# Kernel tuning notes

Measured on AMD Instinct MI355X. Metric: run time of the kernel, lower is better.

The kernel has to match this reference:

```python
import jax, jax.numpy as jnp
import numpy as np

HID, STEM, BN_OUT, STEM_OUT, MLP = 256, 64, 128, 64, 128
BN_WS, STEM_WS = 5, 17
N, H_BN, W_BN, H_VIS, W_VIS = 4096, 128, 128, 1024, 1024


def setup_inputs() -> dict:
    key = jax.random.key(0)
    ks = jax.random.split(key, 24)
    f32 = jnp.float32
    def rn(k, shape, s=0.05):
        return jax.random.normal(k, shape, f32) * s
    return dict(
        bottleneck=rn(ks[0], (1, HID, H_BN, W_BN), 1.0),
        vis_stem_features=rn(ks[1], (1, STEM, H_VIS, W_VIS), 1.0),
        source_positions_vis=jax.random.uniform(ks[2], (N, 2), f32, 10.0, W_VIS - 10.0),
        pixel_to_sky=rn(ks[3], (N, 2, 2), 0.1),
        fused_h=H_BN, fused_w=W_BN, vis_h=H_VIS, vis_w=W_VIS,
        dw_w=rn(ks[4], (HID, 1, 7, 7)), dw_b=rn(ks[5], (HID,)),
        ln_g=jnp.ones((HID,), f32), ln_b=jnp.zeros((HID,), f32),
        pw1_w=rn(ks[6], (4 * HID, HID)), pw1_b=rn(ks[7], (4 * HID,)),
        pw2_w=rn(ks[8], (HID, 4 * HID)), pw2_b=rn(ks[9], (HID,)),
        cn_gamma=jnp.full((HID,), 1e-2, f32),
        bn1x1_w=rn(ks[10], (BN_OUT, HID, 1, 1)), bn1x1_b=rn(ks[11], (BN_OUT,)),
        st1_w=rn(ks[12], (STEM_OUT, STEM, 3, 3)), st1_b=rn(ks[13], (STEM_OUT,)),
        st2_w=rn(ks[14], (STEM_OUT, STEM_OUT, 3, 3)), st2_b=rn(ks[15], (STEM_OUT,)),
        h1_w=rn(ks[16], (MLP, BN_OUT + STEM_OUT)), h1_b=rn(ks[17], (MLP,)),
        h2_w=rn(ks[18], (MLP, MLP)), h2_b=rn(ks[19], (MLP,)),
        h3_w=rn(ks[20], (3, MLP)),
        h3_b=jnp.array([0.0, 0.0, float(np.log(0.05))], f32),
    )


def _gelu(x):
    return jax.nn.gelu(x, approximate=False)


def _conv2d(x, w, b, padding, groups=1):
    y = jax.lax.conv_general_dilated(
        x, w, (1, 1), [(padding, padding), (padding, padding)],
        dimension_numbers=('NCHW', 'OIHW', 'NCHW'), feature_group_count=groups)
    return y + b[None, :, None, None]


def _bilinear_windows(fm, pos, ws):
    """fm [1,C,H,W], pos [N,2] pixel coords -> [N,C,ws,ws].
    Matches torch grid_sample(mode=bilinear, padding=zeros, align_corners=True)
    with the module's normalize/unnormalize, i.e. direct pixel-coord sampling."""
    C, H, W = fm.shape[1:]
    fm2 = fm[0]
    half = ws // 2
    off = jnp.arange(-half, half + 1, dtype=pos.dtype)
    gy, gx = jnp.meshgrid(off, off, indexing='ij')
    xs = gx[None] + pos[:, 0, None, None]   # [N,ws,ws]
    ys = gy[None] + pos[:, 1, None, None]
    x0 = jnp.floor(xs); y0 = jnp.floor(ys)
    wx1 = xs - x0; wy1 = ys - y0
    x0i = x0.astype(jnp.int32); y0i = y0.astype(jnp.int32)
    def gather(yi, xi, w):
        valid = (yi >= 0) & (yi < H) & (xi >= 0) & (xi < W)
        v = fm2[:, jnp.clip(yi, 0, H - 1), jnp.clip(xi, 0, W - 1)]  # [C,N,ws,ws]
        return v * (w * valid)[None]
    out = (gather(y0i, x0i, (1 - wy1) * (1 - wx1))
           + gather(y0i, x0i + 1, (1 - wy1) * wx1)
           + gather(y0i + 1, x0i, wy1 * (1 - wx1))
           + gather(y0i + 1, x0i + 1, wy1 * wx1))
    return jnp.transpose(out, (1, 0, 2, 3))


def _gauss(ws):
    t = jnp.linspace(-1.0, 1.0, ws)
    yy, xx = jnp.meshgrid(t, t, indexing='ij')
    g = jnp.exp(-(xx ** 2 + yy ** 2) / (2 * 0.4 ** 2))
    return g / g.sum()


def _convnext(x, dw_w, dw_b, ln_g, ln_b, pw1_w, pw1_b, pw2_w, pw2_b, gamma):
    r = x
    x = _conv2d(x, dw_w, dw_b, padding=3, groups=x.shape[1])  # depthwise 7x7
    mu = x.mean(1, keepdims=True)
    var = ((x - mu) ** 2).mean(1, keepdims=True)
    x = (x - mu) / jnp.sqrt(var + 1e-6)
    x = x * ln_g[None, :, None, None] + ln_b[None, :, None, None]
    x = jnp.einsum('nchw,oc->nohw', x, pw1_w) + pw1_b[None, :, None, None]
    x = _gelu(x)
    x = jnp.einsum('nchw,oc->nohw', x, pw2_w) + pw2_b[None, :, None, None]
    return r + gamma[None, :, None, None] * x


def _forward(bottleneck, vis_stem_features, source_positions_vis, pixel_to_sky,
             dw_w, dw_b, ln_g, ln_b, pw1_w, pw1_b, pw2_w, pw2_b, cn_gamma,
             bn1x1_w, bn1x1_b, st1_w, st1_b, st2_w, st2_b,
             h1_w, h1_b, h2_w, h2_b, h3_w, h3_b,
             fused_h, fused_w, vis_h, vis_w):
    scale = jnp.array([fused_w / vis_w, fused_h / vis_h], source_positions_vis.dtype)
    pos_bn = source_positions_vis * scale
    # bottleneck branch: 5x5 windows -> ConvNeXt -> 1x1 conv -> GELU -> gauss pool
    bn_win = _bilinear_windows(bottleneck, pos_bn, BN_WS)              # [N,256,5,5]
    bn_feat = _convnext(bn_win, dw_w, dw_b, ln_g, ln_b, pw1_w, pw1_b, pw2_w, pw2_b, cn_gamma)
    bn_feat = _gelu(_conv2d(bn_feat, bn1x1_w, bn1x1_b, padding=0))     # [N,128,5,5]
    bn_vec = (bn_feat * _gauss(BN_WS)[None, None]).sum((-2, -1))       # [N,128]
    st_win = _bilinear_windows(vis_stem_features, source_positions_vis, STEM_WS)
    st = _gelu(_conv2d(st_win, st1_w, st1_b, padding=1))
    st = _gelu(_conv2d(st, st2_w, st2_b, padding=1))                   # [N,64,17,17]
    st_vec = (st * _gauss(STEM_WS)[None, None]).sum((-2, -1))          # [N,64]
    # head MLP
    x = jnp.concatenate([bn_vec, st_vec], axis=1)                      # [N,192]
    x = _gelu(x @ h1_w.T + h1_b)
    x = _gelu(x @ h2_w.T + h2_b)
    out = x @ h3_w.T + h3_b                                            # [N,3]
    dx_px, dy_px = out[:, 0], out[:, 1]
    log_sigma = jnp.clip(out[:, 2], -6.0, 3.0)
    pix = jnp.stack([dx_px, dy_px], axis=1)                            # [N,2]
    pred_sky = jnp.einsum('nij,nj->ni', pixel_to_sky, pix)             # [N,2]
    confidence = 1.0 / jnp.maximum(jnp.exp(log_sigma), 1e-4)
    return pred_sky, dx_px, dy_px, log_sigma, confidence


def reference(bottleneck, vis_stem_features, source_positions_vis, pixel_to_sky,
              fused_h, fused_w, vis_h, vis_w,
              dw_w, dw_b, ln_g, ln_b, pw1_w, pw1_b, pw2_w, pw2_b, cn_gamma,
              bn1x1_w, bn1x1_b, st1_w, st1_b, st2_w, st2_b,
              h1_w, h1_b, h2_w, h2_b, h3_w, h3_b):
    return _forward(bottleneck, vis_stem_features, source_positions_vis, pixel_to_sky,
                    dw_w, dw_b, ln_g, ln_b, pw1_w, pw1_b, pw2_w, pw2_b, cn_gamma,
                    bn1x1_w, bn1x1_b, st1_w, st1_b, st2_w, st2_b,
                    h1_w, h1_b, h2_w, h2_b, h3_w, h3_b,
                    fused_h, fused_w, vis_h, vis_w)
```

## Files before the change

### kernel.cpp

```cpp
#include <hip/hip_runtime.h>
#include <hip/hip_bf16.h>

#define XSTR 28

typedef short short8 __attribute__((ext_vector_type(8)));
typedef float f32x4  __attribute__((ext_vector_type(4)));
typedef float f32x16 __attribute__((ext_vector_type(16)));

__device__ __forceinline__ float gelu_f(float x){
    return 0.5f*x*(1.0f + erff(x*0.70710678118654752f));
}
__device__ __forceinline__ float gelu_q(float x){
    const float z = 1.5957691216057308f*x*(1.0f + 0.044715f*x*x);
    return x / (1.0f + __expf(-z));
}
__device__ __forceinline__ unsigned short f2bf(float f){
    unsigned int u = __float_as_uint(f);
    u += 0x7fffu + ((u>>16)&1u);
    return (unsigned short)(u>>16);
}
__device__ __forceinline__ unsigned int pack2(float a, float b){
    return (unsigned int)f2bf(a) | ((unsigned int)f2bf(b)<<16);
}
__device__ __forceinline__ float bf_lo(unsigned int u){ return __uint_as_float(u<<16); }
__device__ __forceinline__ float bf_hi(unsigned int u){ return __uint_as_float(u & 0xffff0000u); }
__device__ __forceinline__ float bfu(unsigned short v){ return __uint_as_float(((unsigned int)v)<<16); }

__device__ __forceinline__ void fma_row25(const float* __restrict__ row, float w, float* __restrict__ acc){
    const float4* r4 = (const float4*)row;
    float4 a0=r4[0], a1=r4[1], a2=r4[2], a3=r4[3], a4=r4[4], a5=r4[5];
    float a6 = row[24];
    acc[0]+=a0.x*w;  acc[1]+=a0.y*w;  acc[2]+=a0.z*w;  acc[3]+=a0.w*w;
    acc[4]+=a1.x*w;  acc[5]+=a1.y*w;  acc[6]+=a1.z*w;  acc[7]+=a1.w*w;
    acc[8]+=a2.x*w;  acc[9]+=a2.y*w;  acc[10]+=a2.z*w; acc[11]+=a2.w*w;
    acc[12]+=a3.x*w; acc[13]+=a3.y*w; acc[14]+=a3.z*w; acc[15]+=a3.w*w;
    acc[16]+=a4.x*w; acc[17]+=a4.y*w; acc[18]+=a4.z*w; acc[19]+=a4.w*w;
    acc[20]+=a5.x*w; acc[21]+=a5.y*w; acc[22]+=a5.z*w; acc[23]+=a5.w*w;
    acc[24]+=a6*w;
}

__device__ __forceinline__ void bn_body(
    unsigned char* __restrict__ U, int n0, int t,
    const float* __restrict__ bottleneck, const float* __restrict__ pos,
    const float* __restrict__ dw_w, const float* __restrict__ dw_b,
    const float* __restrict__ ln_g, const float* __restrict__ ln_b,
    const float* __restrict__ pw1_b, const float* __restrict__ pw2_b,
    const float* __restrict__ cn_gamma, const float* __restrict__ bn1x1_b,
    const short8* __restrict__ P1v, const short8* __restrict__ P2v,
    const short8* __restrict__ Pbv,
    float* __restrict__ vec_out)
{
    unsigned char* Xb = U;
    unsigned char* Hc = U + 32768;
    float* redA = (float*)(U + 49152);
    float* redB = (float*)(U + 50752);
    float* muS  = (float*)(U + 52352);
    float* rsS  = (float*)(U + 52576);

    const int lane = t & 63, w = t >> 6;
    const int mcol = lane & 15, h4 = lane >> 4;
    const int sP = t >> 8, cP = t & 255;

    unsigned int wvp[13];
    float xdw[25];
    {
        const int n = n0 + sP;
        const float px = pos[2*n]*0.125f, py = pos[2*n+1]*0.125f;
        const float fpx = floorf(px), fpy = floorf(py);
        const int ix0 = (int)fpx - 2, iy0 = (int)fpy - 2;
        const float fx = px - fpx, fy = py - fpy;
        const float w00=(1.f-fy)*(1.f-fx), w01=(1.f-fy)*fx, w10=fy*(1.f-fx), w11=fy*fx;
        float wv[25];
        {
            const float* fm = bottleneck + cP*16384;
            float P[6][6];
            #pragma unroll
            for (int r=0;r<6;r++){
                const int y = iy0+r;
                const bool yok = (y>=0)&&(y<128);
                const int yc = y<0?0:(y>127?127:y);
                #pragma unroll
                for (int s=0;s<6;s++){
                    const int x = ix0+s;
                    const bool ok = yok && (x>=0) && (x<128);
                    const int xc = x<0?0:(x>127?127:x);
                    P[r][s] = ok ? fm[yc*128+xc] : 0.f;
                }
            }
            #pragma unroll
            for (int a=0;a<5;a++)
            #pragma unroll
            for (int b=0;b<5;b++)
                wv[a*5+b] = w00*P[a][b]+w01*P[a][b+1]+w10*P[a+1][b]+w11*P[a+1][b+1];
        }
        #pragma unroll
        for (int i=0;i<12;i++) wvp[i] = pack2(wv[2*i], wv[2*i+1]);
        wvp[12] = pack2(wv[24], 0.f);
        {
            float wcr[49];
            const float* wc = dw_w + cP*49;
            #pragma unroll
            for (int k=0;k<49;k++) wcr[k]=wc[k];
            const float bb = dw_b[cP];
            #pragma unroll
            for (int i=0;i<5;i++){
                #pragma unroll
                for (int j=0;j<5;j++){
                    float a = bb;
                    #pragma unroll
                    for (int u=0;u<7;u++){
                        const int y = i+u-3;
                        if (y<0||y>4) continue;
                        #pragma unroll
                        for (int v=0;v<7;v++){
                            const int x = j+v-3;
                            if (x<0||x>4) continue;
                            a += wv[y*5+x]*wcr[u*7+v];
                        }
                    }
                    xdw[i*5+j] = a;
                }
            }
        }
        #pragma unroll
        for (int p=0;p<25;p++){
            const int row = sP*32 + p;
            *(unsigned short*)(Xb + row*512 + ((2*cP) ^ ((row&7)<<4))) = f2bf(xdw[p]);
        }
    }
    __syncthreads();
    if (t < 400){
        const int sp = t>>3, part = t&7;
        const int row = (sp/25)*32 + (sp - (sp/25)*25);
        float a=0.f, b=0.f;
        for (int c=part; c<256; c+=8){
            const float v = bfu(*(const unsigned short*)(Xb + row*512 + ((2*c) ^ ((row&7)<<4))));
            a += v; b += v*v;
        }
        redA[t]=a; redB[t]=b;
    }
    __syncthreads();
    if (t < 50){
        float a=0.f, b=0.f;
        #pragma unroll
        for (int s=0;s<8;s++){ a+=redA[t*8+s]; b+=redB[t*8+s]; }
        const float m = a*(1.f/256.f);
        const float var = b*(1.f/256.f) - m*m;
        muS[t]=m; rsS[t]=rsqrtf(var+1e-6f);
    }
    __syncthreads();
    {
        const float g = ln_g[cP], bb = ln_b[cP];
        #pragma unroll
        for (int p=0;p<25;p++){
            const int row = sP*32 + p;
            const float v = (xdw[p]-muS[sP*25+p])*rsS[sP*25+p]*g + bb;
            *(unsigned short*)(Xb + row*512 + ((2*cP) ^ ((row&7)<<4))) = f2bf(v);
        }
    }
    __syncthreads();

    f32x4 acc2[2][4];
    #pragma unroll
    for (int ml=0;ml<2;ml++)
        #pragma unroll
        for (int nt=0;nt<4;nt++) acc2[ml][nt]=0.f;

    for (int ch=0; ch<8; ++ch){
        const int mt = ch*8 + w;
        f32x4 a1[4];
        #pragma unroll
        for (int nt=0;nt<4;nt++) a1[nt]=0.f;
        #pragma unroll
        for (int kk=0; kk<8; ++kk){
            const short8 av = P1v[((mt<<3)+kk)*64 + lane];
            #pragma unroll
            for (int nt=0; nt<4; ++nt){
                const int row = nt*16 + mcol;
                const int ad = row*512 + ((kk*64 + h4*16) ^ ((row&7)<<4));
                const short8 bv = *(const short8*)(Xb + ad);
                a1[nt] = __builtin_amdgcn_mfma_f32_16x16x32_bf16(av, bv, a1[nt], 0,0,0);
            }
        }
        {
            const float4 b1v = *(const float4*)(pw1_b + mt*16 + h4*4);
            #pragma unroll
            for (int nt=0; nt<4; ++nt){
                const int row = nt*16 + mcol;
                const float g0 = gelu_q(a1[nt].x + b1v.x);
                const float g1 = gelu_q(a1[nt].y + b1v.y);
                const float g2 = gelu_q(a1[nt].z + b1v.z);
                const float g3 = gelu_q(a1[nt].w + b1v.w);
                const int ad = row*256 + ((w*32 + h4*8) ^ ((row&7)<<4));
                *(uint2*)(Hc + ad) = make_uint2(pack2(g0,g1), pack2(g2,g3));
            }
        }
        __syncthreads();
        #pragma unroll
        for (int ml=0; ml<2; ++ml){
            const int mtc = w*2 + ml;
            #pragma unroll
            for (int kk2=0; kk2<4; ++kk2){
                const short8 av = P2v[(mtc*32 + (ch*4 + kk2))*64 + lane];
                #pragma unroll
                for (int nt=0; nt<4; ++nt){
                    const int row = nt*16 + mcol;
                    const int ad = row*256 + ((kk2*64 + h4*16) ^ ((row&7)<<4));
                    const short8 bv = *(const short8*)(Hc + ad);
                    acc2[ml][nt] = __builtin_amdgcn_mfma_f32_16x16x32_bf16(av, bv, acc2[ml][nt], 0,0,0);
                }
            }
        }
        __syncthreads();
    }

    #pragma unroll
    for (int ml=0; ml<2; ++ml){
        const int c0 = (w*2+ml)*16 + h4*4;
        const float4 gm = *(const float4*)(cn_gamma + c0);
        const float4 b2 = *(const float4*)(pw2_b + c0);
        #pragma unroll
        for (int nt=0; nt<4; ++nt){
            const int row = nt*16 + mcol;
            const int ad = row*512 + ((2*c0) ^ ((row&7)<<4));
            const float f0 = gm.x*(acc2[ml][nt].x + b2.x);
            const float f1 = gm.y*(acc2[ml][nt].y + b2.y);
            const float f2 = gm.z*(acc2[ml][nt].z + b2.z);
            const float f3 = gm.w*(acc2[ml][nt].w + b2.w);
            *(uint2*)(Xb + ad) = make_uint2(pack2(f0,f1), pack2(f2,f3));
        }
    }
    __syncthreads();
    #pragma unroll
    for (int p=0;p<25;p++){
        const int row = sP*32 + p;
        unsigned short* ptr = (unsigned short*)(Xb + row*512 + ((2*cP) ^ ((row&7)<<4)));
        const float r = (p&1) ? bf_hi(wvp[p>>1]) : bf_lo(wvp[p>>1]);
        *ptr = f2bf(bfu(*ptr) + r);
    }
    __syncthreads();

    {
        f32x4 a3[4];
        #pragma unroll
        for (int nt=0;nt<4;nt++) a3[nt]=0.f;
        #pragma unroll
        for (int kk=0; kk<8; ++kk){
            const short8 av = Pbv[((w<<3)+kk)*64 + lane];
            #pragma unroll
            for (int nt=0; nt<4; ++nt){
                const int row = nt*16 + mcol;
                const int ad = row*512 + ((kk*64 + h4*16) ^ ((row&7)<<4));
                const short8 bv = *(const short8*)(Xb + ad);
                a3[nt] = __builtin_amdgcn_mfma_f32_16x16x32_bf16(av, bv, a3[nt], 0,0,0);
            }
        }
        const float4 bb = *(const float4*)(bn1x1_b + w*16 + h4*4);
        float e5[5];
        #pragma unroll
        for (int a=0;a<5;a++){
            const float ta = -1.f + 0.5f*a;
            e5[a] = expf(-3.125f*ta*ta);
        }
        const float Sv = e5[0]+e5[1]+e5[2]+e5[3]+e5[4];
        const float invS = 1.0f/(Sv*Sv);
        float sA[2][4];
        #pragma unroll
        for (int s=0;s<2;s++)
            #pragma unroll
            for (int j=0;j<4;j++) sA[s][j]=0.f;
        #pragma unroll
        for (int nt=0; nt<4; ++nt){
            const int row = nt*16 + mcol;
            const int s = row>>5, p = row&31;
            if (p < 25){
                const int pa = p/5, pb = p - pa*5;
                const float g = e5[pa]*e5[pb];
                sA[s][0] += g*gelu_q(a3[nt].x + bb.x);
                sA[s][1] += g*gelu_q(a3[nt].y + bb.y);
                sA[s][2] += g*gelu_q(a3[nt].z + bb.z);
                sA[s][3] += g*gelu_q(a3[nt].w + bb.w);
            }
        }
        #pragma unroll
        for (int off=1; off<16; off<<=1){
            #pragma unroll
            for (int s=0;s<2;s++)
                #pragma unroll
                for (int j=0;j<4;j++) sA[s][j] += __shfl_xor(sA[s][j], off);
        }
        if (mcol == 0){
            const int o = w*16 + h4*4;
            #pragma unroll
            for (int s=0;s<2;s++){
                float* vo = vec_out + (n0+s)*192 + o;
                vo[0]=sA[s][0]*invS; vo[1]=sA[s][1]*invS;
                vo[2]=sA[s][2]*invS; vo[3]=sA[s][3]*invS;
            }
        }
    }
}

#define STEM_CONV32(SRC, AP)                                                        \
    _Pragma("unroll")                                                               \
    for (int k=0;k<9;k++){                                                          \
        int tj[3];                                                                  \
        _Pragma("unroll")                                                           \
        for (int j=0;j<3;j++)                                                       \
            tj[j] = (int)sTab[m*90 + (j<cnt ? st+j : st)*9 + k];                    \
        _Pragma("unroll")                                                           \
        for (int kt=0;kt<4;kt++){                                                   \
            const short8 av = (AP)[(k*8 + kt*2 + wo)*64 + lane];                    \
            const int cb = kt*32 + hi16;                                            \
            _Pragma("unroll")                                                       \
            for (int j=0;j<3;j++){                                                  \
                if (j < cnt){                                                       \
                    const short8 bv = *(const short8*)((SRC) + (tj[j] ^ cb));       \
                    acc[j] = __builtin_amdgcn_mfma_f32_32x32x16_bf16(av, bv, acc[j], 0,0,0); \
                }                                                                   \
            }                                                                       \
        }                                                                           \
    }

__device__ __forceinline__ void stem_body(
    unsigned char* __restrict__ U, int n, int t,
    const float* __restrict__ vis, const float* __restrict__ pos,
    const short8* __restrict__ Ap1,
    const float* __restrict__ st1_b, const float* __restrict__ st2_b,
    float* __restrict__ vec_out)
{
    unsigned char* sXt = U;
    unsigned short* sTab = (unsigned short*)(U + 37120);
    float (*redS)[4] = (float(*)[4])(U + 42880);

    const int lane = t & 63;
    const int m = lane & 31;
    const int hi = lane >> 5;
    const int hi16 = hi*16;
    const int w = t >> 6;
    const int wo = w & 1;
    const int nh = w >> 1;
    const int st  = nh*3 - (nh==3 ? 1 : 0);
    const int cnt = (nh < 2) ? 3 : 2;

    const float fpx0 = pos[2*n], fpy0 = pos[2*n+1];
    const float fpx = floorf(fpx0), fpy = floorf(fpy0);
    const int ix0 = (int)fpx - 8, iy0 = (int)fpy - 8;
    const float fx = fpx0-fpx, fy = fpy0-fpy;
    const float w00=(1.f-fy)*(1.f-fx), w01=(1.f-fy)*fx, w10=fy*(1.f-fx), w11=fy*fx;

    if (t < 32) *(unsigned int*)(sXt + 289*128 + t*4) = 0u;

    for (int idx = t; idx < 32*90; idx += 512){
        const int mm = idx/90, rem = idx - mm*90;
        const int nt = rem/9, k = rem - nt*9;
        const int p = nt*32 + mm;
        int pp = 289;
        if (p < 289){
            const int py = (p*241)>>12, px = p - py*17;
            const int y = py + k/3 - 1, x = px + (k - (k/3)*3) - 1;
            if (((unsigned)y < 17u) && ((unsigned)x < 17u)) pp = y*17 + x;
        }
        sTab[idx] = (unsigned short)(pp*128 + ((pp&7)<<4));
    }

    for (int task = t; task < 64*17; task += 512){
        const int c  = task & 63;
        const int py = task >> 6;
        const float* r0 = vis + c*1048576 + (iy0+py)*1024 + ix0;
        float a[18], b[18];
        #pragma unroll
        for (int kk=0; kk<18; kk++){ a[kk]=r0[kk]; b[kk]=r0[1024+kk]; }
        #pragma unroll
        for (int px=0; px<17; px++){
            const float v = w00*a[px] + w01*a[px+1] + w10*b[px] + w11*b[px+1];
            const int p = py*17 + px;
            *(unsigned short*)(sXt + p*128 + ((2*c) ^ ((p&7)<<4))) = f2bf(v);
        }
    }
    __syncthreads();

    f32x16 acc[3];
    #pragma unroll
    for (int j=0;j<3;j++) acc[j] = 0.f;
    STEM_CONV32(sXt, Ap1)

    uint2 pk[3][4];
    {
        float4 b4[4];
        #pragma unroll
        for (int rg=0;rg<4;rg++) b4[rg] = *(const float4*)(st1_b + wo*32 + 8*rg + 4*hi);
        #pragma unroll
        for (int j=0;j<3;j++){
            if (j < cnt){
                #pragma unroll
                for (int rg=0;rg<4;rg++){
                    const float v0 = gelu_q(acc[j][4*rg+0] + b4[rg].x);
                    const float v1 = gelu_q(acc[j][4*rg+1] + b4[rg].y);
                    const float v2 = gelu_q(acc[j][4*rg+2] + b4[rg].z);
                    const float v3 = gelu_q(acc[j][4*rg+3] + b4[rg].w);
                    pk[j][rg] = make_uint2(pack2(v0,v1), pack2(v2,v3));
                }
            }
        }
    }
    __syncthreads();

    #pragma unroll
    for (int j=0;j<3;j++){
        if (j < cnt){
            const int p = (st+j)*32 + m;
            if (p < 289){
                const int swz = (p&7)<<4;
                #pragma unroll
                for (int rg=0;rg<4;rg++){
                    const int ch0 = wo*32 + 8*rg + 4*hi;
                    *(uint2*)(sXt + p*128 + ((2*ch0) ^ swz)) = pk[j][rg];
                }
            }
        }
    }
    __syncthreads();

    const short8* Ap2 = Ap1 + 4608;
    #pragma unroll
    for (int j=0;j<3;j++) acc[j] = 0.f;
    STEM_CONV32(sXt, Ap2)

    {
        float4 b4[4];
        #pragma unroll
        for (int rg=0;rg<4;rg++) b4[rg] = *(const float4*)(st2_b + wo*32 + 8*rg + 4*hi);
        float s[16];
        #pragma unroll
        for (int r=0;r<16;r++) s[r]=0.f;
        #pragma unroll
        for (int j=0;j<3;j++){
            if (j < cnt){
                const int p = (st+j)*32 + m;
                if (p < 289){
                    const int py = (p*241)>>12;
                    const int px = p - py*17;
                    const float ty = -1.f + 0.125f*py;
                    const float tx = -1.f + 0.125f*px;
                    const float g = expf(-3.125f*(ty*ty + tx*tx));
                    #pragma unroll
                    for (int rg=0;rg<4;rg++){
                        s[4*rg+0] += g*gelu_q(acc[j][4*rg+0] + b4[rg].x);
                        s[4*rg+1] += g*gelu_q(acc[j][4*rg+1] + b4[rg].y);
                        s[4*rg+2] += g*gelu_q(acc[j][4*rg+2] + b4[rg].z);
                        s[4*rg+3] += g*gelu_q(acc[j][4*rg+3] + b4[rg].w);
                    }
                }
            }
        }
        #pragma unroll
        for (int off=1; off<32; off<<=1){
            #pragma unroll
            for (int r=0;r<16;r++) s[r] += __shfl_xor(s[r], off);
        }
        if (m == 0){
            #pragma unroll
            for (int rg=0;rg<4;rg++)
                #pragma unroll
                for (int e=0;e<4;e++)
                    redS[wo*32 + 8*rg + 4*hi + e][nh] = s[4*rg+e];
        }
    }
    __syncthreads();
    if (t < 64){
        float Sv = 0.f;
        #pragma unroll
        for (int j=0;j<17;j++){
            const float tj = -1.f + 0.125f*j;
            Sv += expf(-3.125f*tj*tj);
        }
        vec_out[n*192+128+t] = (redS[t][0] + redS[t][1] + redS[t][2] + redS[t][3]) / (Sv*Sv);
    }
}

__global__ __launch_bounds__(512,4) void fused_branches(
    const float* __restrict__ bottleneck, const float* __restrict__ vis,
    const float* __restrict__ pos,
    const float* __restrict__ dw_w, const float* __restrict__ dw_b,
    const float* __restrict__ ln_g, const float* __restrict__ ln_b,
    const float* __restrict__ pw1_b, const float* __restrict__ pw2_b,
    const float* __restrict__ cn_gamma, const float* __restrict__ bn1x1_b,
    const short8* __restrict__ P1v, const short8* __restrict__ P2v,
    const short8* __restrict__ Pbv,
    const short8* __restrict__ Ap1,
    const float* __restrict__ st1_b, const float* __restrict__ st2_b,
    float* __restrict__ vec_out)
{
    __shared__ __align__(16) unsigned char U[52800];
    const int b = blockIdx.x, t = threadIdx.x;
    const int q = b/3, r = b - q*3;
    if (r == 0){
        bn_body(U, q*2, t, bottleneck, pos, dw_w, dw_b, ln_g, ln_b,
                pw1_b, pw2_b, cn_gamma, bn1x1_b, P1v, P2v, Pbv, vec_out);
    } else {
        stem_body(U, q*2 + r - 1, t, vis, pos, Ap1, st1_b, st2_b, vec_out);
    }
}

__global__ __launch_bounds__(256) void prepack_bn_kernel(
    const float* __restrict__ W1, const float* __restrict__ W2, const float* __restrict__ Wb,
    unsigned short* __restrict__ P1, unsigned short* __restrict__ P2, unsigned short* __restrict__ Pb)
{
    const int tid = blockIdx.x*256 + threadIdx.x;
    const float* src; unsigned short* dst; int row, col, stride, idx;
    if (tid < 32768){
        idx = tid;
        const int frag = idx>>6, l = idx&63;
        row = (frag>>3)*16 + (l&15); col = (frag&7)*32 + (l>>4)*8; stride = 256;
        src = W1; dst = P1;
    } else if (tid < 65536){
        idx = tid - 32768;
        const int frag = idx>>6, l = idx&63;
        row = (frag>>5)*16 + (l&15); col = (frag&31)*32 + (l>>4)*8; stride = 1024;
        src = W2; dst = P2;
    } else if (tid < 69632){
        idx = tid - 65536;
        const int frag = idx>>6, l = idx&63;
        row = (frag>>3)*16 + (l&15); col = (frag&7)*32 + (l>>4)*8; stride = 256;
        src = Wb; dst = Pb;
    } else return;
    const float* s = src + row*stride + col;
    unsigned int v[4];
    #pragma unroll
    for (int j=0;j<4;j++) v[j] = pack2(s[2*j], s[2*j+1]);
    *(uint4*)(dst + (size_t)idx*8) = make_uint4(v[0],v[1],v[2],v[3]);
}

__global__ __launch_bounds__(256,2) void bn_branch_valu(
    const float* __restrict__ bottleneck, const float* __restrict__ pos,
    const float* __restrict__ dw_w, const float* __restrict__ dw_b,
    const float* __restrict__ ln_g, const float* __restrict__ ln_b,
    const float* __restrict__ pw1_w, const float* __restrict__ pw1_b,
    const float* __restrict__ pw2_w, const float* __restrict__ pw2_b,
    const float* __restrict__ cn_gamma,
    const float* __restrict__ bn1x1_w, const float* __restrict__ bn1x1_b,
    float* __restrict__ vec_out)
{
    __shared__ float xln[256*XSTR];
    __shared__ float hbuf[256*XSTR];
    __shared__ float redA[200], redB[200];
    __shared__ float mu[25], rs[25];

    const int n = blockIdx.x;
    const int t = threadIdx.x;
    const int c = t;

    const float px = pos[2*n]*0.125f, py = pos[2*n+1]*0.125f;
    const float fpx = floorf(px), fpy = floorf(py);
    const int ix0 = (int)fpx - 2, iy0 = (int)fpy - 2;
    const float fx = px - fpx, fy = py - fpy;
    const float w00=(1.f-fy)*(1.f-fx), w01=(1.f-fy)*fx, w10=fy*(1.f-fx), w11=fy*fx;

    float wv[25];
    {
        const float* fm = bottleneck + c*16384;
        float P[6][6];
        #pragma unroll
        for (int r=0;r<6;r++){
            const int y = iy0+r;
            const bool yok = (y>=0)&&(y<128);
            const int yc = y<0?0:(y>127?127:y);
            #pragma unroll
            for (int s=0;s<6;s++){
                const int x = ix0+s;
                const bool ok = yok && (x>=0) && (x<128);
                const int xc = x<0?0:(x>127?127:x);
                P[r][s] = ok ? fm[yc*128+xc] : 0.f;
            }
        }
        #pragma unroll
        for (int a=0;a<5;a++)
        #pragma unroll
        for (int b=0;b<5;b++)
            wv[a*5+b] = w00*P[a][b]+w01*P[a][b+1]+w10*P[a+1][b]+w11*P[a+1][b+1];
    }
    {
        float wcr[49];
        const float* wc = dw_w + c*49;
        #pragma unroll
        for (int k=0;k<49;k++) wcr[k]=wc[k];
        const float bb = dw_b[c];
        #pragma unroll
        for (int i=0;i<5;i++){
            #pragma unroll
            for (int j=0;j<5;j++){
                float a = bb;
                #pragma unroll
                for (int u=0;u<7;u++){
                    const int y = i+u-3;
                    if (y<0||y>4) continue;
                    #pragma unroll
                    for (int v=0;v<7;v++){
                        const int x = j+v-3;
                        if (x<0||x>4) continue;
                        a += wv[y*5+x]*wcr[u*7+v];
                    }
                }
                xln[c*XSTR + i*5+j] = a;
            }
        }
    }
    __syncthreads();
    if (t < 200){
        const int p = t>>3, s = t&7;
        float a=0.f, b=0.f;
        for (int cc=s; cc<256; cc+=8){
            const float v = xln[cc*XSTR+p];
            a += v; b += v*v;
        }
        redA[t]=a; redB[t]=b;
    }
    __syncthreads();
    if (t < 25){
        float a=0.f, b=0.f;
        #pragma unroll
        for (int s=0;s<8;s++){ a+=redA[t*8+s]; b+=redB[t*8+s]; }
        const float m = a*(1.f/256.f);
        const float var = b*(1.f/256.f) - m*m;
        mu[t]=m; rs[t]=rsqrtf(var+1e-6f);
    }
    __syncthreads();
    {
        const float g = ln_g[c], bb = ln_b[c];
        #pragma unroll
        for (int p=0;p<25;p++)
            xln[c*XSTR+p] = (xln[c*XSTR+p]-mu[p])*rs[p]*g + bb;
    }
    __syncthreads();
    float acc2[25];
    #pragma unroll
    for (int p=0;p<25;p++) acc2[p]=0.f;
    for (int r=0;r<4;r++){
        const int o = r*256 + t;
        float h[25];
        {
            const float b1 = pw1_b[o];
            #pragma unroll
            for (int p=0;p<25;p++) h[p]=b1;
            const float* wr = pw1_w + o*256;
            for (int cc=0;cc<256;cc++)
                fma_row25(xln + cc*XSTR, wr[cc], h);
            #pragma unroll
            for (int p=0;p<25;p++) h[p]=gelu_f(h[p]);
        }
        __syncthreads();
        #pragma unroll
        for (int p=0;p<25;p++) hbuf[t*XSTR+p]=h[p];
        __syncthreads();
        {
            const float* w2 = pw2_w + t*1024 + r*256;
            for (int k=0;k<256;k++)
                fma_row25(hbuf + k*XSTR, w2[k], acc2);
        }
    }
    {
        const float gam = cn_gamma[c], b2 = pw2_b[c];
        #pragma unroll
        for (int p=0;p<25;p++)
            xln[c*XSTR+p] = wv[p] + gam*(acc2[p]+b2);
    }
    __syncthreads();
    if (t < 128){
        float acc[25];
        #pragma unroll
        for (int p=0;p<25;p++) acc[p]=0.f;
        const float* wr = bn1x1_w + t*256;
        for (int cc=0;cc<256;cc++)
            fma_row25(xln + cc*XSTR, wr[cc], acc);
        const float b = bn1x1_b[t];
        float e5[5];
        #pragma unroll
        for (int a=0;a<5;a++){
            const float ta = -1.f + 0.5f*a;
            e5[a] = expf(-3.125f*ta*ta);
        }
        const float Sv = e5[0]+e5[1]+e5[2]+e5[3]+e5[4];
        float res = 0.f;
        #pragma unroll
        for (int a=0;a<5;a++){
            float rowa = 0.f;
            #pragma unroll
            for (int bb=0;bb<5;bb++)
                rowa += e5[bb]*gelu_f(acc[a*5+bb]+b);
            res += e5[a]*rowa;
        }
        vec_out[n*192+t] = res/(Sv*Sv);
    }
}

__global__ __launch_bounds__(256) void prepack_kernel(
    const float* __restrict__ W1, const float* __restrict__ W2,
    unsigned short* __restrict__ Ap)
{
    const int tid = blockIdx.x*256 + threadIdx.x;
    if (tid >= 9216) return;
    const int conv = tid / 4608;
    const int r = tid - conv*4608;
    const int frag = r >> 6, l = r & 63;
    const int k  = frag >> 3;
    const int kt = (frag >> 1) & 3;
    const int wo = frag & 1;
    const float* W = conv ? W2 : W1;
    const int o  = wo*32 + (l & 31);
    const int c0 = kt*16 + (l >> 5)*8;
    unsigned int v[4];
    #pragma unroll
    for (int jj=0; jj<4; jj++){
        const float f0 = W[o*576 + (c0+2*jj  )*9 + k];
        const float f1 = W[o*576 + (c0+2*jj+1)*9 + k];
        v[jj] = pack2(f0, f1);
    }
    *(uint4*)(Ap + (size_t)tid*8) = make_uint4(v[0], v[1], v[2], v[3]);
}

__global__ __launch_bounds__(512,4) void stem_branch_kernel(
    const float* __restrict__ vis,
    const float* __restrict__ pos,
    const short8* __restrict__ Ap1,
    const float* __restrict__ st1_b,
    const float* __restrict__ st2_b,
    float* __restrict__ vec_out)
{
    __shared__ __align__(16) unsigned char U[43904];
    stem_body(U, blockIdx.x, threadIdx.x, vis, pos, Ap1, st1_b, st2_b, vec_out);
}

__global__ __launch_bounds__(128) void head16_kernel(
    const float* __restrict__ vec, const float* __restrict__ p2s,
    const float* __restrict__ h1_w, const float* __restrict__ h1_b,
    const float* __restrict__ h2_w, const float* __restrict__ h2_b,
    const float* __restrict__ h3_w, const float* __restrict__ h3_b,
    float* __restrict__ out, int N)
{
    __shared__ float v[16][192];
    __shared__ float x1s[16][132];
    __shared__ float x2s[16][132];
    __shared__ float o3s[16][4];
    const int n0 = blockIdx.x*16, t = threadIdx.x;

    for (int idx=t; idx<16*192; idx+=128){
        const int s = idx/192, k = idx - s*192;
        v[s][k] = vec[n0*192 + idx];
    }
    __syncthreads();
    {
        const int o = t;
        float acc[16];
        const float b = h1_b[o];
        #pragma unroll
        for (int s=0;s<16;s++) acc[s]=b;
        const float4* wr = (const float4*)(h1_w + o*192);
        for (int k4=0;k4<48;k4++){
            const float4 wv4 = wr[k4];
            #pragma unroll
            for (int s=0;s<16;s++){
                const float4 vv = *(const float4*)&v[s][k4*4];
                acc[s] += wv4.x*vv.x + wv4.y*vv.y + wv4.z*vv.z + wv4.w*vv.w;
            }
        }
        #pragma unroll
        for (int s=0;s<16;s++) x1s[s][o] = gelu_f(acc[s]);
    }
    __syncthreads();
    {
        const int o = t;
        float acc[16];
        const float b = h2_b[o];
        #pragma unroll
        for (int s=0;s<16;s++) acc[s]=b;
        const float4* wr = (const float4*)(h2_w + o*128);
        for (int k4=0;k4<32;k4++){
            const float4 wv4 = wr[k4];
            #pragma unroll
            for (int s=0;s<16;s++){
                const float4 vv = *(const float4*)&x1s[s][k4*4];
                acc[s] += wv4.x*vv.x + wv4.y*vv.y + wv4.z*vv.z + wv4.w*vv.w;
            }
        }
        #pragma unroll
        for (int s=0;s<16;s++) x2s[s][o] = gelu_f(acc[s]);
    }
    __syncthreads();
    if (t < 48){
        const int j = t>>4, s = t&15;
        float a = h3_b[j];
        const float* wr = h3_w + j*128;
        for (int k=0;k<128;k++) a += x2s[s][k]*wr[k];
        o3s[s][j] = a;
    }
    __syncthreads();
    if (t < 16){
        const int s = t, n = n0 + s;
        const float dx = o3s[s][0], dy = o3s[s][1];
        float ls = o3s[s][2];
        ls = ls < -6.f ? -6.f : (ls > 3.f ? 3.f : ls);
        const float s0 = p2s[n*4+0]*dx + p2s[n*4+1]*dy;
        const float s1 = p2s[n*4+2]*dx + p2s[n*4+3]*dy;
        const float conf = 1.0f/fmaxf(expf(ls), 1e-4f);
        out[2*n]   = s0;
        out[2*n+1] = s1;
        out[2*N+n] = dx;
        out[3*N+n] = dy;
        out[4*N+n] = ls;
        out[5*N+n] = conf;
    }
}

extern "C" void kernel_launch(void* const* d_in, const int* in_sizes, int n_in,
                              void* d_out, int out_size, void* d_ws, size_t ws_size,
                              hipStream_t stream)
{
    (void)n_in; (void)out_size;
    const float* bottleneck = (const float*)d_in[0];
    const float* vis        = (const float*)d_in[1];
    const float* pos        = (const float*)d_in[2];
    const float* p2s        = (const float*)d_in[3];
    const float* dw_w  = (const float*)d_in[8];
    const float* dw_b  = (const float*)d_in[9];
    const float* ln_g  = (const float*)d_in[10];
    const float* ln_b  = (const float*)d_in[11];
    const float* pw1_w = (const float*)d_in[12];
    const float* pw1_b = (const float*)d_in[13];
    const float* pw2_w = (const float*)d_in[14];
    const float* pw2_b = (const float*)d_in[15];
    const float* gam   = (const float*)d_in[16];
    const float* b1w   = (const float*)d_in[17];
    const float* b1b   = (const float*)d_in[18];
    const float* s1w   = (const float*)d_in[19];
    const float* s1b   = (const float*)d_in[20];
    const float* s2w   = (const float*)d_in[21];
    const float* s2b   = (const float*)d_in[22];
    const float* h1w   = (const float*)d_in[23];
    const float* h1b   = (const float*)d_in[24];
    const float* h2w   = (const float*)d_in[25];
    const float* h2b   = (const float*)d_in[26];
    const float* h3w   = (const float*)d_in[27];
    const float* h3b   = (const float*)d_in[28];

    const int N = in_sizes[2]/2;
    float* vec = (float*)d_ws;
    const size_t vec_bytes = (size_t)N*192*sizeof(float);
    unsigned short* Apack = (unsigned short*)((char*)d_ws + vec_bytes);
    unsigned short* P1 = Apack + 73728;
    unsigned short* P2 = P1 + 262144;
    unsigned short* Pb = P2 + 262144;
    const size_t need = vec_bytes + 147456u + (262144u+262144u+32768u)*2u;

    hipMemsetAsync(d_ws, 0, vec_bytes, stream);

    prepack_kernel<<<36, 256, 0, stream>>>(s1w, s2w, Apack);

    if (ws_size >= need){
        prepack_bn_kernel<<<272, 256, 0, stream>>>(pw1_w, pw2_w, b1w, P1, P2, Pb);
        fused_branches<<<3*(N/2), 512, 0, stream>>>(bottleneck, vis, pos,
                                                    dw_w, dw_b, ln_g, ln_b,
                                                    pw1_b, pw2_b, gam, b1b,
                                                    (const short8*)P1, (const short8*)P2, (const short8*)Pb,
                                                    (const short8*)Apack, s1b, s2b, vec);
    } else {
        bn_branch_valu<<<N, 256, 0, stream>>>(bottleneck, pos, dw_w, dw_b, ln_g, ln_b,
                                              pw1_w, pw1_b, pw2_w, pw2_b, gam, b1w, b1b, vec);
        stem_branch_kernel<<<N, 512, 0, stream>>>(vis, pos, (const short8*)Apack, s1b, s2b, vec);
    }
    head16_kernel<<<N/16, 128, 0, stream>>>(vec, p2s, h1w, h1b, h2w, h2b, h3w, h3b,
                                            (float*)d_out, N);
}
```

Before: 869.3 us.

## Pre-transpose vis stem features to channel-last bf16 and split fused kernel

Adds a kernel that converts the full 64x1024x1024 vis feature map into a channel-last bf16 copy, so each stem block gathers its 17x17 bilinear window with 16-byte vector loads instead of strided per-channel fp32 reads. The combined bottleneck/stem launch is split back into separate stem and bottleneck kernels. The trade is an extra full-map pass (256MB read, 128MB write) and a 128MB workspace requirement; the fast path only runs if the workspace is large enough. Bilinear inputs are now bf16-rounded before interpolation, which adds a little rounding error.

```diff
diff --git a/kernel.cpp b/kernel.cpp
--- a/kernel.cpp
+++ b/kernel.cpp
@@ -301,206 +301,19 @@
     }
 }
 
-#define STEM_CONV32(SRC, AP)                                                        \
-    _Pragma("unroll")                                                               \
-    for (int k=0;k<9;k++){                                                          \
-        int tj[3];                                                                  \
-        _Pragma("unroll")                                                           \
-        for (int j=0;j<3;j++)                                                       \
-            tj[j] = (int)sTab[m*90 + (j<cnt ? st+j : st)*9 + k];                    \
-        _Pragma("unroll")                                                           \
-        for (int kt=0;kt<4;kt++){                                                   \
-            const short8 av = (AP)[(k*8 + kt*2 + wo)*64 + lane];                    \
-            const int cb = kt*32 + hi16;                                            \
-            _Pragma("unroll")                                                       \
-            for (int j=0;j<3;j++){                                                  \
-                if (j < cnt){                                                       \
-                    const short8 bv = *(const short8*)((SRC) + (tj[j] ^ cb));       \
-                    acc[j] = __builtin_amdgcn_mfma_f32_32x32x16_bf16(av, bv, acc[j], 0,0,0); \
-                }                                                                   \
-            }                                                                       \
-        }                                                                           \
-    }
-
-__device__ __forceinline__ void stem_body(
-    unsigned char* __restrict__ U, int n, int t,
-    const float* __restrict__ vis, const float* __restrict__ pos,
-    const short8* __restrict__ Ap1,
-    const float* __restrict__ st1_b, const float* __restrict__ st2_b,
-    float* __restrict__ vec_out)
-{
-    unsigned char* sXt = U;
-    unsigned short* sTab = (unsigned short*)(U + 37120);
-    float (*redS)[4] = (float(*)[4])(U + 42880);
-
-    const int lane = t & 63;
-    const int m = lane & 31;
-    const int hi = lane >> 5;
-    const int hi16 = hi*16;
-    const int w = t >> 6;
-    const int wo = w & 1;
-    const int nh = w >> 1;
-    const int st  = nh*3 - (nh==3 ? 1 : 0);
-    const int cnt = (nh < 2) ? 3 : 2;
-
-    const float fpx0 = pos[2*n], fpy0 = pos[2*n+1];
-    const float fpx = floorf(fpx0), fpy = floorf(fpy0);
-    const int ix0 = (int)fpx - 8, iy0 = (int)fpy - 8;
-    const float fx = fpx0-fpx, fy = fpy0-fpy;
-    const float w00=(1.f-fy)*(1.f-fx), w01=(1.f-fy)*fx, w10=fy*(1.f-fx), w11=fy*fx;
-
-    if (t < 32) *(unsigned int*)(sXt + 289*128 + t*4) = 0u;
-
-    for (int idx = t; idx < 32*90; idx += 512){
-        const int mm = idx/90, rem = idx - mm*90;
-        const int nt = rem/9, k = rem - nt*9;
-        const int p = nt*32 + mm;
-        int pp = 289;
-        if (p < 289){
-            const int py = (p*241)>>12, px = p - py*17;
-            const int y = py + k/3 - 1, x = px + (k - (k/3)*3) - 1;
-            if (((unsigned)y < 17u) && ((unsigned)x < 17u)) pp = y*17 + x;
-        }
-        sTab[idx] = (unsigned short)(pp*128 + ((pp&7)<<4));
-    }
-
-    for (int task = t; task < 64*17; task += 512){
-        const int c  = task & 63;
-        const int py = task >> 6;
-        const float* r0 = vis + c*1048576 + (iy0+py)*1024 + ix0;
-        float a[18], b[18];
-        #pragma unroll
-        for (int kk=0; kk<18; kk++){ a[kk]=r0[kk]; b[kk]=r0[1024+kk]; }
-        #pragma unroll
-        for (int px=0; px<17; px++){
-            const float v = w00*a[px] + w01*a[px+1] + w10*b[px] + w11*b[px+1];
-            const int p = py*17 + px;
-            *(unsigned short*)(sXt + p*128 + ((2*c) ^ ((p&7)<<4))) = f2bf(v);
-        }
-    }
-    __syncthreads();
-
-    f32x16 acc[3];
-    #pragma unroll
-    for (int j=0;j<3;j++) acc[j] = 0.f;
-    STEM_CONV32(sXt, Ap1)
-
-    uint2 pk[3][4];
-    {
-        float4 b4[4];
-        #pragma unroll
-        for (int rg=0;rg<4;rg++) b4[rg] = *(const float4*)(st1_b + wo*32 + 8*rg + 4*hi);
-        #pragma unroll
-        for (int j=0;j<3;j++){
-            if (j < cnt){
-                #pragma unroll
-                for (int rg=0;rg<4;rg++){
-                    const float v0 = gelu_q(acc[j][4*rg+0] + b4[rg].x);
-                    const float v1 = gelu_q(acc[j][4*rg+1] + b4[rg].y);
-                    const float v2 = gelu_q(acc[j][4*rg+2] + b4[rg].z);
-                    const float v3 = gelu_q(acc[j][4*rg+3] + b4[rg].w);
-                    pk[j][rg] = make_uint2(pack2(v0,v1), pack2(v2,v3));
-                }
-            }
-        }
-    }
-    __syncthreads();
-
-    #pragma unroll
-    for (int j=0;j<3;j++){
-        if (j < cnt){
-            const int p = (st+j)*32 + m;
-            if (p < 289){
-                const int swz = (p&7)<<4;
-                #pragma unroll
-                for (int rg=0;rg<4;rg++){
-                    const int ch0 = wo*32 + 8*rg + 4*hi;
-                    *(uint2*)(sXt + p*128 + ((2*ch0) ^ swz)) = pk[j][rg];
-                }
-            }
-        }
-    }
-    __syncthreads();
-
-    const short8* Ap2 = Ap1 + 4608;
-    #pragma unroll
-    for (int j=0;j<3;j++) acc[j] = 0.f;
-    STEM_CONV32(sXt, Ap2)
-
-    {
-        float4 b4[4];
-        #pragma unroll
-        for (int rg=0;rg<4;rg++) b4[rg] = *(const float4*)(st2_b + wo*32 + 8*rg + 4*hi);
-        float s[16];
-        #pragma unroll
-        for (int r=0;r<16;r++) s[r]=0.f;
-        #pragma unroll
-        for (int j=0;j<3;j++){
-            if (j < cnt){
-                const int p = (st+j)*32 + m;
-                if (p < 289){
-                    const int py = (p*241)>>12;
-                    const int px = p - py*17;
-                    const float ty = -1.f + 0.125f*py;
-                    const float tx = -1.f + 0.125f*px;
-                    const float g = expf(-3.125f*(ty*ty + tx*tx));
-                    #pragma unroll
-                    for (int rg=0;rg<4;rg++){
-                        s[4*rg+0] += g*gelu_q(acc[j][4*rg+0] + b4[rg].x);
-                        s[4*rg+1] += g*gelu_q(acc[j][4*rg+1] + b4[rg].y);
-                        s[4*rg+2] += g*gelu_q(acc[j][4*rg+2] + b4[rg].z);
-                        s[4*rg+3] += g*gelu_q(acc[j][4*rg+3] + b4[rg].w);
-                    }
-                }
-            }
-        }
-        #pragma unroll
-        for (int off=1; off<32; off<<=1){
-            #pragma unroll
-            for (int r=0;r<16;r++) s[r] += __shfl_xor(s[r], off);
-        }
-        if (m == 0){
-            #pragma unroll
-            for (int rg=0;rg<4;rg++)
-                #pragma unroll
-                for (int e=0;e<4;e++)
-                    redS[wo*32 + 8*rg + 4*hi + e][nh] = s[4*rg+e];
-        }
-    }
-    __syncthreads();
-    if (t < 64){
-        float Sv = 0.f;
-        #pragma unroll
-        for (int j=0;j<17;j++){
-            const float tj = -1.f + 0.125f*j;
-            Sv += expf(-3.125f*tj*tj);
-        }
-        vec_out[n*192+128+t] = (redS[t][0] + redS[t][1] + redS[t][2] + redS[t][3]) / (Sv*Sv);
-    }
-}
-
-__global__ __launch_bounds__(512,4) void fused_branches(
-    const float* __restrict__ bottleneck, const float* __restrict__ vis,
-    const float* __restrict__ pos,
+__global__ __launch_bounds__(512,4) void bn_branch_mfma(
+    const float* __restrict__ bottleneck, const float* __restrict__ pos,
     const float* __restrict__ dw_w, const float* __restrict__ dw_b,
     const float* __restrict__ ln_g, const float* __restrict__ ln_b,
     const float* __restrict__ pw1_b, const float* __restrict__ pw2_b,
     const float* __restrict__ cn_gamma, const float* __restrict__ bn1x1_b,
     const short8* __restrict__ P1v, const short8* __restrict__ P2v,
     const short8* __restrict__ Pbv,
-    const short8* __restrict__ Ap1,
-    const float* __restrict__ st1_b, const float* __restrict__ st2_b,
     float* __restrict__ vec_out)
 {
     __shared__ __align__(16) unsigned char U[52800];
-    const int b = blockIdx.x, t = threadIdx.x;
-    const int q = b/3, r = b - q*3;
-    if (r == 0){
-        bn_body(U, q*2, t, bottleneck, pos, dw_w, dw_b, ln_g, ln_b,
-                pw1_b, pw2_b, cn_gamma, bn1x1_b, P1v, P2v, Pbv, vec_out);
-    } else {
-        stem_body(U, q*2 + r - 1, t, vis, pos, Ap1, st1_b, st2_b, vec_out);
-    }
+    bn_body(U, blockIdx.x*2, threadIdx.x, bottleneck, pos, dw_w, dw_b, ln_g, ln_b,
+            pw1_b, pw2_b, cn_gamma, bn1x1_b, P1v, P2v, Pbv, vec_out);
 }
 
 __global__ __launch_bounds__(256) void prepack_bn_kernel(
@@ -719,16 +532,256 @@
     *(uint4*)(Ap + (size_t)tid*8) = make_uint4(v[0], v[1], v[2], v[3]);
 }
 
-__global__ __launch_bounds__(512,4) void stem_branch_kernel(
-    const float* __restrict__ vis,
+__global__ __launch_bounds__(256) void transpose_vis_kernel(
+    const float* __restrict__ vis, unsigned short* __restrict__ visT)
+{
+    __shared__ unsigned short T[64*66];
+    const int b = blockIdx.x;
+    const int y = b >> 4, x0 = (b & 15) << 6;
+    const int t = threadIdx.x, lane = t & 63, w = t >> 6;
+    #pragma unroll
+    for (int i = 0; i < 16; ++i){
+        const int c = w*16 + i;
+        T[c*66 + lane] = f2bf(vis[c*1048576 + y*1024 + x0 + lane]);
+    }
+    __syncthreads();
+    const int x = t >> 2, cg0 = (t & 3) * 16;
+    #pragma unroll
+    for (int h = 0; h < 2; ++h){
+        const int cg = cg0 + h*8;
+        unsigned int v[4];
+        #pragma unroll
+        for (int j = 0; j < 4; ++j){
+            const unsigned int a = T[(cg + 2*j    )*66 + x];
+            const unsigned int bsh = T[(cg + 2*j + 1)*66 + x];
+            v[j] = a | (bsh << 16);
+        }
+        *(uint4*)(visT + ((size_t)(y*1024) + x0 + x)*64 + cg) = make_uint4(v[0],v[1],v[2],v[3]);
+    }
+}
+
+#define STEM_CONV32(SRC, AP)                                                        \
+    _Pragma("unroll")                                                               \
+    for (int k=0;k<9;k++){                                                          \
+        int tj[3];                                                                  \
+        _Pragma("unroll")                                                           \
+        for (int j=0;j<3;j++)                                                       \
+            tj[j] = (int)sTab[m*90 + (j<cnt ? st+j : st)*9 + k];                    \
+        _Pragma("unroll")                                                           \
+        for (int kt=0;kt<4;kt++){                                                   \
+            const short8 av = (AP)[(k*8 + kt*2 + wo)*64 + lane];                    \
+            const int cb = kt*32 + hi16;                                            \
+            _Pragma("unroll")                                                       \
+            for (int j=0;j<3;j++){                                                  \
+                if (j < cnt){                                                       \
+                    const short8 bv = *(const short8*)((SRC) + (tj[j] ^ cb));       \
+                    acc[j] = __builtin_amdgcn_mfma_f32_32x32x16_bf16(av, bv, acc[j], 0,0,0); \
+                }                                                                   \
+            }                                                                       \
+        }                                                                           \
+    }
+
+template<bool TR>
+__device__ __forceinline__ void stem_body(
+    unsigned char* __restrict__ U, int n, int t,
+    const float* __restrict__ vis, const unsigned short* __restrict__ visT,
     const float* __restrict__ pos,
     const short8* __restrict__ Ap1,
-    const float* __restrict__ st1_b,
-    const float* __restrict__ st2_b,
+    const float* __restrict__ st1_b, const float* __restrict__ st2_b,
     float* __restrict__ vec_out)
 {
+    unsigned char* sXt = U;
+    unsigned short* sTab = (unsigned short*)(U + 37120);
+    float (*redS)[4] = (float(*)[4])(U + 42880);
+
+    const int lane = t & 63;
+    const int m = lane & 31;
+    const int hi = lane >> 5;
+    const int hi16 = hi*16;
+    const int w = t >> 6;
+    const int wo = w & 1;
+    const int nh = w >> 1;
+    const int st  = nh*3 - (nh==3 ? 1 : 0);
+    const int cnt = (nh < 2) ? 3 : 2;
+
+    const float fpx0 = pos[2*n], fpy0 = pos[2*n+1];
+    const float fpx = floorf(fpx0), fpy = floorf(fpy0);
+    const int ix0 = (int)fpx - 8, iy0 = (int)fpy - 8;
+    const float fx = fpx0-fpx, fy = fpy0-fpy;
+    const float w00=(1.f-fy)*(1.f-fx), w01=(1.f-fy)*fx, w10=fy*(1.f-fx), w11=fy*fx;
+
+    if (t < 32) *(unsigned int*)(sXt + 289*128 + t*4) = 0u;
+
+    for (int idx = t; idx < 32*90; idx += 512){
+        const int mm = idx/90, rem = idx - mm*90;
+        const int nt = rem/9, k = rem - nt*9;
+        const int p = nt*32 + mm;
+        int pp = 289;
+        if (p < 289){
+            const int py = (p*241)>>12, px = p - py*17;
+            const int y = py + k/3 - 1, x = px + (k - (k/3)*3) - 1;
+            if (((unsigned)y < 17u) && ((unsigned)x < 17u)) pp = y*17 + x;
+        }
+        sTab[idx] = (unsigned short)(pp*128 + ((pp&7)<<4));
+    }
+
+    if (TR){
+        for (int idx = t; idx < 289*8; idx += 512){
+            const int p = idx >> 3, cg = (idx & 7) * 8;
+            const int py = (p*241)>>12, px = p - py*17;
+            const unsigned short* q = visT + (size_t)((iy0+py)*1024 + (ix0+px))*64 + cg;
+            const uint4 q00 = *(const uint4*)(q);
+            const uint4 q01 = *(const uint4*)(q + 64);
+            const uint4 q10 = *(const uint4*)(q + 65536);
+            const uint4 q11 = *(const uint4*)(q + 65536 + 64);
+            unsigned int o[4];
+            #pragma unroll
+            for (int j=0;j<4;j++){
+                const unsigned int u00=((const unsigned int*)&q00)[j];
+                const unsigned int u01=((const unsigned int*)&q01)[j];
+                const unsigned int u10=((const unsigned int*)&q10)[j];
+                const unsigned int u11=((const unsigned int*)&q11)[j];
+                const float lo = bf_lo(u00)*w00 + bf_lo(u01)*w01 + bf_lo(u10)*w10 + bf_lo(u11)*w11;
+                const float hv = bf_hi(u00)*w00 + bf_hi(u01)*w01 + bf_hi(u10)*w10 + bf_hi(u11)*w11;
+                o[j] = pack2(lo, hv);
+            }
+            *(uint4*)(sXt + p*128 + ((2*cg) ^ ((p&7)<<4))) = make_uint4(o[0],o[1],o[2],o[3]);
+        }
+    } else {
+        for (int task = t; task < 64*17; task += 512){
+            const int c  = task & 63;
+            const int py = task >> 6;
+            const float* r0 = vis + c*1048576 + (iy0+py)*1024 + ix0;
+            float a[18], b[18];
+            #pragma unroll
+            for (int kk=0; kk<18; kk++){ a[kk]=r0[kk]; b[kk]=r0[1024+kk]; }
+            #pragma unroll
+            for (int px=0; px<17; px++){
+                const float v = w00*a[px] + w01*a[px+1] + w10*b[px] + w11*b[px+1];
+                const int p = py*17 + px;
+                *(unsigned short*)(sXt + p*128 + ((2*c) ^ ((p&7)<<4))) = f2bf(v);
+            }
+        }
+    }
+    __syncthreads();
+
+    f32x16 acc[3];
+    #pragma unroll
+    for (int j=0;j<3;j++) acc[j] = 0.f;
+    STEM_CONV32(sXt, Ap1)
+
+    uint2 pk[3][4];
+    {
+        float4 b4[4];
+        #pragma unroll
+        for (int rg=0;rg<4;rg++) b4[rg] = *(const float4*)(st1_b + wo*32 + 8*rg + 4*hi);
+        #pragma unroll
+        for (int j=0;j<3;j++){
+            if (j < cnt){
+                #pragma unroll
+                for (int rg=0;rg<4;rg++){
+                    const float v0 = gelu_q(acc[j][4*rg+0] + b4[rg].x);
+                    const float v1 = gelu_q(acc[j][4*rg+1] + b4[rg].y);
+                    const float v2 = gelu_q(acc[j][4*rg+2] + b4[rg].z);
+                    const float v3 = gelu_q(acc[j][4*rg+3] + b4[rg].w);
+                    pk[j][rg] = make_uint2(pack2(v0,v1), pack2(v2,v3));
+                }
+            }
+        }
+    }
+    __syncthreads();
+
+    #pragma unroll
+    for (int j=0;j<3;j++){
+        if (j < cnt){
+            const int p = (st+j)*32 + m;
+            if (p < 289){
+                const int swz = (p&7)<<4;
+                #pragma unroll
+                for (int rg=0;rg<4;rg++){
+                    const int ch0 = wo*32 + 8*rg + 4*hi;
+                    *(uint2*)(sXt + p*128 + ((2*ch0) ^ swz)) = pk[j][rg];
+                }
+            }
+        }
+    }
+    __syncthreads();
+
+    const short8* Ap2 = Ap1 + 4608;
+    #pragma unroll
+    for (int j=0;j<3;j++) acc[j] = 0.f;
+    STEM_CONV32(sXt, Ap2)
+
+    {
+        float4 b4[4];
+        #pragma unroll
+        for (int rg=0;rg<4;rg++) b4[rg] = *(const float4*)(st2_b + wo*32 + 8*rg + 4*hi);
+        float s[16];
+        #pragma unroll
+        for (int r=0;r<16;r++) s[r]=0.f;
+        #pragma unroll
+        for (int j=0;j<3;j++){
+            if (j < cnt){
+                const int p = (st+j)*32 + m;
+                if (p < 289){
+                    const int py = (p*241)>>12;
+                    const int px = p - py*17;
+                    const float ty = -1.f + 0.125f*py;
+                    const float tx = -1.f + 0.125f*px;
+                    const float g = expf(-3.125f*(ty*ty + tx*tx));
+                    #pragma unroll
+                    for (int rg=0;rg<4;rg++){
+                        s[4*rg+0] += g*gelu_q(acc[j][4*rg+0] + b4[rg].x);
+                        s[4*rg+1] += g*gelu_q(acc[j][4*rg+1] + b4[rg].y);
+                        s[4*rg+2] += g*gelu_q(acc[j][4*rg+2] + b4[rg].z);
+                        s[4*rg+3] += g*gelu_q(acc[j][4*rg+3] + b4[rg].w);
+                    }
+                }
+            }
+        }
+        #pragma unroll
+        for (int off=1; off<32; off<<=1){
+            #pragma unroll
+            for (int r=0;r<16;r++) s[r] += __shfl_xor(s[r], off);
+        }
+        if (m == 0){
+            #pragma unroll
+            for (int rg=0;rg<4;rg++)
+                #pragma unroll
+                for (int e=0;e<4;e++)
+                    redS[wo*32 + 8*rg + 4*hi + e][nh] = s[4*rg+e];
+        }
+    }
+    __syncthreads();
+    if (t < 64){
+        float Sv = 0.f;
+        #pragma unroll
+        for (int j=0;j<17;j++){
+            const float tj = -1.f + 0.125f*j;
+            Sv += expf(-3.125f*tj*tj);
+        }
+        vec_out[n*192+128+t] = (redS[t][0] + redS[t][1] + redS[t][2] + redS[t][3]) / (Sv*Sv);
+    }
+}
+
+__global__ __launch_bounds__(512,4) void stem_kernel_tr(
+    const unsigned short* __restrict__ visT, const float* __restrict__ pos,
+    const short8* __restrict__ Ap1,
+    const float* __restrict__ st1_b, const float* __restrict__ st2_b,
+    float* __restrict__ vec_out)
+{
     __shared__ __align__(16) unsigned char U[43904];
-    stem_body(U, blockIdx.x, threadIdx.x, vis, pos, Ap1, st1_b, st2_b, vec_out);
+    stem_body<true>(U, blockIdx.x, threadIdx.x, nullptr, visT, pos, Ap1, st1_b, st2_b, vec_out);
+}
+
+__global__ __launch_bounds__(512,4) void stem_branch_kernel(
+    const float* __restrict__ vis, const float* __restrict__ pos,
+    const short8* __restrict__ Ap1,
+    const float* __restrict__ st1_b, const float* __restrict__ st2_b,
+    float* __restrict__ vec_out)
+{
+    __shared__ __align__(16) unsigned char U[43904];
+    stem_body<false>(U, blockIdx.x, threadIdx.x, vis, nullptr, pos, Ap1, st1_b, st2_b, vec_out);
 }
 
 __global__ __launch_bounds__(128) void head16_kernel(
@@ -844,25 +897,35 @@
     const float* h3b   = (const float*)d_in[28];
 
     const int N = in_sizes[2]/2;
-    float* vec = (float*)d_ws;
+    char* ws = (char*)d_ws;
+    float* vec = (float*)ws;
+    unsigned short* Apack = (unsigned short*)(ws + 3145728);
+    unsigned short* P1    = (unsigned short*)(ws + 3293184);
+    unsigned short* P2    = (unsigned short*)(ws + 3817472);
+    unsigned short* Pb    = (unsigned short*)(ws + 4341760);
+    unsigned short* visT  = (unsigned short*)(ws + 4407296);
+    const size_t need_mfma = 4407296u;
+    const size_t need_tr   = 4407296u + 134217728ull;
     const size_t vec_bytes = (size_t)N*192*sizeof(float);
-    unsigned short* Apack = (unsigned short*)((char*)d_ws + vec_bytes);
-    unsigned short* P1 = Apack + 73728;
-    unsigned short* P2 = P1 + 262144;
-    unsigned short* Pb = P2 + 262144;
-    const size_t need = vec_bytes + 147456u + (262144u+262144u+32768u)*2u;
 
     hipMemsetAsync(d_ws, 0, vec_bytes, stream);
-
     prepack_kernel<<<36, 256, 0, stream>>>(s1w, s2w, Apack);
 
-    if (ws_size >= need){
+    if (ws_size >= need_tr){
         prepack_bn_kernel<<<272, 256, 0, stream>>>(pw1_w, pw2_w, b1w, P1, P2, Pb);
-        fused_branches<<<3*(N/2), 512, 0, stream>>>(bottleneck, vis, pos,
-                                                    dw_w, dw_b, ln_g, ln_b,
-                                                    pw1_b, pw2_b, gam, b1b,
-                                                    (const short8*)P1, (const short8*)P2, (const short8*)Pb,
-                                                    (const short8*)Apack, s1b, s2b, vec);
+        transpose_vis_kernel<<<16384, 256, 0, stream>>>(vis, visT);
+        stem_kernel_tr<<<N, 512, 0, stream>>>(visT, pos, (const short8*)Apack, s1b, s2b, vec);
+        bn_branch_mfma<<<N/2, 512, 0, stream>>>(bottleneck, pos, dw_w, dw_b, ln_g, ln_b,
+                                                pw1_b, pw2_b, gam, b1b,
+                                                (const short8*)P1, (const short8*)P2, (const short8*)Pb,
+                                                vec);
+    } else if (ws_size >= need_mfma){
+        prepack_bn_kernel<<<272, 256, 0, stream>>>(pw1_w, pw2_w, b1w, P1, P2, Pb);
+        bn_branch_mfma<<<N/2, 512, 0, stream>>>(bottleneck, pos, dw_w, dw_b, ln_g, ln_b,
+                                                pw1_b, pw2_b, gam, b1b,
+                                                (const short8*)P1, (const short8*)P2, (const short8*)Pb,
+                                                vec);
+        stem_branch_kernel<<<N, 512, 0, stream>>>(vis, pos, (const short8*)Apack, s1b, s2b, vec);
     } else {
         bn_branch_valu<<<N, 256, 0, stream>>>(bottleneck, pos, dw_w, dw_b, ln_g, ln_b,
                                               pw1_w, pw1_b, pw2_w, pw2_b, gam, b1w, b1b, vec);
```

Result: faster. 776.3 us (-10.7%).
